# Performance work log

Measured on AMD Instinct MI355X. Metric: run time of the kernel, lower is better.

The kernel has to match this reference:

```python
import jax
jax.config.update('jax_enable_x64', True)  # exact int64 phase products (torch builds phasors in complex128)
import jax.numpy as jnp
import numpy as np

L = 393216          # seq_length, divisible by Locc=4, K=12, mmse_block=12
K = 12              # ktc=4 -> K=12
LOCC = 4            # _compute_locc for ktc=4
U, P = 8, 4         # max_users, max_ports_per_user
BLK = 12            # mmse_block_size
SEARCH_MIN, SEARCH_MAX = -10, 10


def setup_inputs() -> dict:
    key = jax.random.key(0)
    k1, k2, k3 = jax.random.split(key, 3)
    ls_real = jax.random.normal(k1, (L,), dtype=jnp.float32)
    ls_imag = jax.random.normal(k2, (L,), dtype=jnp.float32)
    cyclic_shifts = jax.random.randint(k3, (U, P), 0, K)  # int, values in [0, K)
    return {"ls_real": ls_real, "ls_imag": ls_imag, "cyclic_shifts": cyclic_shifts}


def _phasor(m):
    """exp(1j*2*pi*m*n/L) for each m in the [UP] vector -> [UP, L] complex64.
    Phase reduced mod L in exact int64 before float conversion for accuracy."""
    n = jnp.arange(L, dtype=jnp.int64)
    r = (m.astype(jnp.int64)[:, None] * n[None, :]) % L      # exact
    ang = (2.0 * np.pi / L) * r.astype(jnp.float32)
    return jnp.exp(1j * ang).astype(jnp.complex64)


def _forward(ls, cyclic_shifts):
    shifts = cyclic_shifts.reshape(-1)                        # [UP]
    ideal_peak = ((K - shifts) % K) * L // K                  # [UP]

    # --- timing offset search in +/-10 window around ideal peak (CIR domain) ---
    h_time = jnp.fft.ifft(ls)                                 # IDFT
    h_mag = jnp.abs(h_time) ** 2                              # [L]
    offs = jnp.arange(SEARCH_MIN, SEARCH_MAX + 1)             # [21]
    win = (ideal_peak[:, None] + offs[None, :]) % L           # [UP, 21]
    T = offs[jnp.argmax(h_mag[win], axis=1)]                  # [UP] timing offsets
    m = T + ideal_peak                                        # [UP]

    ph_m = _phasor(m)                                         # [UP, L]
    ph_T = _phasor(T)                                         # [UP, L]

    # --- per-port cyclic de-shift, OCC demux (avg of 4), linear interp back to L ---
    h_up = ls[None, :] * ph_m                                 # [UP, L]
    h_avg = h_up.reshape(-1, L // LOCC, LOCC).mean(-1)        # [UP, L/4]
    orig_idx = (LOCC - 1) / 2.0 + LOCC * jnp.arange(L // LOCC, dtype=jnp.float32)
    new_idx = jnp.arange(L, dtype=jnp.float32)
    interp1 = jax.vmap(lambda y: jnp.interp(new_idx, orig_idx, y))
    h_interp = (interp1(h_avg.real.astype(jnp.float32))
                + 1j * interp1(h_avg.imag.astype(jnp.float32))).astype(jnp.complex64)  # [UP, L]

    # --- residual reconstruction and re-addition per port ---
    h_recon = jnp.sum(h_interp * jnp.conj(ph_m), axis=0)      # [L]
    residual = ls - h_recon
    h_wr = h_interp + residual[None, :] * ph_m                # [UP, L]

    # --- noise power estimate from adjacent-sample differences ---
    diff = ls[1:] - ls[:-1]
    noise_power = jnp.mean(jnp.abs(diff) ** 2) / 2

    # --- block MMSE: h_mmse = C (C + R)^-1 h with default C = I, R = sigma^2 I ---
    C = jnp.eye(BLK, dtype=jnp.complex64)
    Rm = noise_power.astype(jnp.complex64) * jnp.eye(BLK, dtype=jnp.complex64)
    M = C @ jnp.linalg.inv(C + Rm)                            # [12, 12]
    hb = h_wr.reshape(-1, L // BLK, BLK)                      # [UP, L/12, 12]
    h_mmse = jnp.einsum('ij,ubj->ubi', M, hb).reshape(-1, L)  # [UP, L]

    # --- align back by conj timing phasor ---
    return h_mmse * jnp.conj(ph_T)                            # [UP, L] complex64


def reference(ls_real, ls_imag, cyclic_shifts):
    ls = (ls_real + 1j * ls_imag).astype(jnp.complex64)
    return _forward(ls, cyclic_shifts)
```

## Files before the change

kernel.cpp:

```cpp
#include <hip/hip_runtime.h>
#include <math.h>

#define L_TOT 393216
#define L_D4  98304
#define NPORT 32
#define NPEAK 12
#define NOFF  21
#define NCAND 252
#define TILE  1536
#define NBLK  (L_TOT / TILE)
#define NSLOT 12
#define HALF_ELEMS 12582912ull

__device__ float2 g_F[NBLK * NCAND];
__device__ double g_npart[NBLK];
__device__ int    g_prm[96];
__device__ float  g_scale[1];

__constant__ double c_cos12[12] = {1.0, 0.8660254037844387, 0.5, 0.0, -0.5,
  -0.8660254037844387, -1.0, -0.8660254037844387, -0.5, 0.0, 0.5, 0.8660254037844387};
__constant__ double c_sin12[12] = {0.0, 0.5, 0.8660254037844387, 1.0,
  0.8660254037844387, 0.5, 0.0, -0.5, -0.8660254037844387, -1.0,
  -0.8660254037844387, -0.5};

__device__ __forceinline__ void interp_coords(int n, int* j0, float* f) {
  float x = ((float)n - 1.5f) * 0.25f;
  if (x <= 0.f)                    { *j0 = 0;        *f = 0.f; }
  else if (x >= (float)(L_D4 - 1)) { *j0 = L_D4 - 2; *f = 1.f; }
  else { int jj = (int)x; *j0 = jj; *f = x - (float)jj; }
}

__device__ __forceinline__ float2 zpowS(float2 z, float2 z2, float2 z4, float2 z8, int T) {
  int t = T < 0 ? -T : T;
  float cr = 1.f, ci = 0.f;
  if (t & 1) { cr = z.x; ci = z.y; }
  if (t & 2) { float a = cr*z2.x - ci*z2.y, b = cr*z2.y + ci*z2.x; cr = a; ci = b; }
  if (t & 4) { float a = cr*z4.x - ci*z4.y, b = cr*z4.y + ci*z4.x; cr = a; ci = b; }
  if (t & 8) { float a = cr*z8.x - ci*z8.y, b = cr*z8.y + ci*z8.x; cr = a; ci = b; }
  if (T < 0) ci = -ci;
  return make_float2(cr, ci);
}

__global__ __launch_bounds__(256) void search_kernel(
    const float* __restrict__ lsr, const float* __restrict__ lsi) {
  __shared__ float2 sh_ls[TILE + 1];
  __shared__ float2 sh_z[TILE];
  __shared__ float2 sh_red[NCAND * NOFF];
  const float w = (float)(2.0 * M_PI / (double)L_TOT);
  int tid = threadIdx.x;
  int KB = blockIdx.x * TILE;
  for (int i = tid; i < TILE + 1; i += 256) {
    int k = KB + i; if (k > L_TOT - 1) k = L_TOT - 1;
    sh_ls[i] = make_float2(lsr[k], lsi[k]);
  }
  for (int i = tid; i < TILE; i += 256) {
    float s, c; __sincosf(w * (float)(KB + i), &s, &c);
    sh_z[i] = make_float2(c, s);
  }
  __syncthreads();

  if (tid < NCAND) {
    int r = tid % 12, lane = tid / 12;
    float accr[NOFF], acci[NOFF];
#pragma unroll
    for (int d = 0; d < NOFF; ++d) { accr[d] = 0.f; acci[d] = 0.f; }
    for (int q = lane; q < TILE / 12; q += 21) {
      int kl = 12 * q + r;
      float2 y = sh_ls[kl];
      float2 z = sh_z[kl];
      accr[10] += y.x; acci[10] += y.y;
      float cpr = y.x, cpi = y.y, cmr = y.x, cmi = y.y;
#pragma unroll
      for (int d = 1; d <= 10; ++d) {
        float tr = cpr*z.x - cpi*z.y, ti = cpr*z.y + cpi*z.x; cpr = tr; cpi = ti;
        accr[10 + d] += cpr; acci[10 + d] += cpi;
        tr = cmr*z.x + cmi*z.y; ti = cmi*z.x - cmr*z.y; cmr = tr; cmi = ti;
        accr[10 - d] += cmr; acci[10 - d] += cmi;
      }
    }
#pragma unroll
    for (int d = 0; d < NOFF; ++d)
      sh_red[tid * NOFF + d] = make_float2(accr[d], acci[d]);
  }
  double nacc = 0.0;
  int top = (KB + TILE <= L_TOT - 1) ? TILE : (L_TOT - 1 - KB);
  for (int i = tid; i < top; i += 256) {
    float2 a = sh_ls[i], b = sh_ls[i + 1];
    float dr = b.x - a.x, di = b.y - a.y;
    nacc += (double)(dr * dr + di * di);
  }
  __syncthreads();
  if (tid < NCAND) {
    int r = tid / NOFF, dd = tid - r * NOFF;
    float fr = 0.f, fi = 0.f;
    for (int lane = 0; lane < 21; ++lane) {
      float2 v = sh_red[(lane * 12 + r) * NOFF + dd];
      fr += v.x; fi += v.y;
    }
    g_F[blockIdx.x * NCAND + tid] = make_float2(fr, fi);
  }
  __syncthreads();
  double* nb = (double*)sh_red;
  nb[tid] = nacc;
  __syncthreads();
  for (int t = 128; t > 0; t >>= 1) {
    if (tid < t) nb[tid] += nb[tid + t];
    __syncthreads();
  }
  if (tid == 0) g_npart[blockIdx.x] = nb[0];
}

__global__ __launch_bounds__(256) void select_kernel(
    const int* __restrict__ shifts) {
  __shared__ double sGr[NCAND], sGi[NCAND];
  __shared__ double hmag[NCAND];
  __shared__ double nred[256];
  __shared__ int    sh_pu[NPORT], sh_Tu[NPORT];
  int tid = threadIdx.x;
  if (tid < NCAND) {
    double gr = 0.0, gi = 0.0;
    for (int b = 0; b < NBLK; ++b) {
      float2 v = g_F[b * NCAND + tid];
      gr += (double)v.x; gi += (double)v.y;
    }
    sGr[tid] = gr; sGi[tid] = gi;
  }
  nred[tid] = g_npart[tid];
  __syncthreads();
  if (tid < NCAND) {
    int p = tid / NOFF, dd = tid - p * NOFF;
    double sr = 0.0, si = 0.0;
    for (int r = 0; r < 12; ++r) {
      int idx = (p * r) % 12;
      double gr = sGr[r * NOFF + dd], gi = sGi[r * NOFF + dd];
      sr += c_cos12[idx] * gr - c_sin12[idx] * gi;
      si += c_cos12[idx] * gi + c_sin12[idx] * gr;
    }
    hmag[tid] = sr * sr + si * si;
  }
  __syncthreads();
  for (int t = 128; t > 0; t >>= 1) {
    if (tid < t) nred[tid] += nred[tid + t];
    __syncthreads();
  }
  if (tid < NPORT) {
    int s = shifts[tid];
    int p = (NPEAK - (s % NPEAK)) % NPEAK;
    double best = -1.0; int bd = 0;
    for (int d = 0; d < NOFF; ++d) {
      double v = hmag[p * NOFF + d];
      if (v > best) { best = v; bd = d; }
    }
    sh_pu[tid] = p;
    sh_Tu[tid] = bd - 10;
  }
  __syncthreads();
  if (tid == 0) {
    int nd = 0;
    int pv[NSLOT], tv[NSLOT], mv[NSLOT], cv[NSLOT]; unsigned msk[NSLOT];
#pragma unroll
    for (int s = 0; s < NSLOT; ++s) { pv[s] = 0; tv[s] = 0; mv[s] = 0; cv[s] = 0; msk[s] = 0u; }
    for (int u = 0; u < NPORT; ++u) {
      int p = sh_pu[u];
      int slot = -1;
      for (int s = 0; s < nd; ++s) if (pv[s] == p) { slot = s; break; }
      if (slot < 0) {
        slot = nd++;
        pv[slot] = p; tv[slot] = sh_Tu[u];
        int m = sh_Tu[u] + p * (L_TOT / NPEAK);
        if (m < 0) m += L_TOT;
        mv[slot] = m;
      }
      cv[slot] += 1;
      msk[slot] |= (1u << u);
    }
    g_prm[0] = nd;
#pragma unroll
    for (int s = 0; s < NSLOT; ++s) {
      g_prm[1 + s]  = pv[s];
      g_prm[13 + s] = tv[s];
      g_prm[25 + s] = mv[s];
      g_prm[37 + s] = cv[s];
      g_prm[49 + s] = (int)msk[s];
    }
    double npow = nred[0] / (double)(L_TOT - 1) * 0.5;
    g_scale[0] = (float)(1.0 / (1.0 + npow));
  }
}

__global__ __launch_bounds__(256) void fused_kernel(
    const float* __restrict__ lsr, const float* __restrict__ lsi,
    float* __restrict__ out, unsigned long long out_elems) {
  __shared__ float2 sh_ls[264];
  __shared__ float2 sh_h[16][67];
  __shared__ float2 sh_tbl[144];
  __shared__ float2 sh_stp1[NSLOT];
  __shared__ int    sm_T[NSLOT], sm_p[NSLOT], sm_m[NSLOT], sm_cnt[NSLOT], sm_msk[NSLOT];
  __shared__ int    sm_nd;
  __shared__ float  sm_scale;

  const float w = (float)(2.0 * M_PI / (double)L_TOT);
  int tid = threadIdx.x;
  int N0 = blockIdx.x * 256;
  int JBASE; float fd;
  interp_coords(N0, &JBASE, &fd);
  int K0 = 4 * JBASE;

  if (tid < NSLOT) {
    sm_T[tid] = g_prm[13 + tid];
    sm_p[tid] = g_prm[1 + tid];
    int m = g_prm[25 + tid]; sm_m[tid] = m;
    sm_cnt[tid] = g_prm[37 + tid];
    sm_msk[tid] = g_prm[49 + tid];
    float s, c; __sincosf(w * (float)m, &s, &c);
    sh_stp1[tid] = make_float2(c, s);
  }
  if (tid == 0) { sm_nd = g_prm[0]; sm_scale = g_scale[0]; }
  if (tid < 144) {
    int p = tid / 12, r = tid - p * 12;
    int idx = (p * r) % 12;
    float s, c; __sincosf((float)(2.0 * M_PI / 12.0) * (float)idx, &s, &c);
    sh_tbl[tid] = make_float2(c, s);
  }
  for (int i = tid; i < 264; i += 256) {
    int k = K0 + i; if (k > L_TOT - 1) k = L_TOT - 1;
    sh_ls[i] = make_float2(lsr[k], lsi[k]);
  }
  __syncthreads();

  int nd = __builtin_amdgcn_readfirstlane(sm_nd);

  for (int e = tid; e < 66 * 16; e += 256) {
    int s = e & 15, jj = e >> 4;
    if (s < nd) {
      int j = JBASE + jj; if (j > L_D4 - 1) j = L_D4 - 1;
      int k0 = 4 * j, kk = k0 - K0;
      unsigned rr = (unsigned)(((long long)sm_m[s] * k0) % L_TOT);
      float phs, phc; __sincosf(w * (float)rr, &phs, &phc);
      float2 stp = sh_stp1[s];
      float sr = 0.f, si = 0.f;
#pragma unroll
      for (int t = 0; t < 4; ++t) {
        float2 v = sh_ls[kk + t];
        sr += v.x * phc - v.y * phs;
        si += v.x * phs + v.y * phc;
        float a = phc * stp.x - phs * stp.y, b = phc * stp.y + phs * stp.x;
        phc = a; phs = b;
      }
      sh_h[s][jj] = make_float2(0.25f * sr, 0.25f * si);
    }
  }
  __syncthreads();

  int n = N0 + tid;
  int j0; float f;
  interp_coords(n, &j0, &f);
  int jj0 = j0 - JBASE;
  int r12 = n % 12;
  float2 lsn = sh_ls[n - K0];
  float zs, zc; __sincosf(w * (float)n, &zs, &zc);
  float2 zn = make_float2(zc, zs);
  float2 z2 = make_float2(zn.x*zn.x - zn.y*zn.y, 2.f*zn.x*zn.y);
  float2 z4 = make_float2(z2.x*z2.x - z2.y*z2.y, 2.f*z2.x*z2.y);
  float2 z8 = make_float2(z4.x*z4.x - z4.y*z4.y, 2.f*z4.x*z4.y);

  float aAr[NSLOT], aAi[NSLOT];
  float rcr = 0.f, rci = 0.f;
#pragma unroll
  for (int s = 0; s < NSLOT; ++s) {
    if (s < nd) {
      int T = __builtin_amdgcn_readfirstlane(sm_T[s]);
      int p = __builtin_amdgcn_readfirstlane(sm_p[s]);
      float cnt = (float)__builtin_amdgcn_readfirstlane(sm_cnt[s]);
      float2 zT = zpowS(zn, z2, z4, z8, T);
      float2 tb = sh_tbl[p * 12 + r12];
      float2 y0 = sh_h[s][jj0], y1 = sh_h[s][jj0 + 1];
      float hr = y0.x + f * (y1.x - y0.x);
      float hi = y0.y + f * (y1.y - y0.y);
      float Ar = hr * zT.x + hi * zT.y;
      float Ai = hi * zT.x - hr * zT.y;
      aAr[s] = Ar; aAi[s] = Ai;
      rcr += cnt * (Ar * tb.x + Ai * tb.y);
      rci += cnt * (Ai * tb.x - Ar * tb.y);
    } else { aAr[s] = 0.f; aAi[s] = 0.f; }
  }
  float resr = lsn.x - rcr, resi = lsn.y - rci;
  float scl = sm_scale;

  bool full = (out_elems >= 2ull * HALF_ELEMS);
#pragma unroll
  for (int s = 0; s < NSLOT; ++s) {
    if (s < nd) {
      int p = __builtin_amdgcn_readfirstlane(sm_p[s]);
      unsigned mask = (unsigned)__builtin_amdgcn_readfirstlane(sm_msk[s]);
      float2 tb = sh_tbl[p * 12 + r12];
      float orr = scl * (aAr[s] + resr * tb.x - resi * tb.y);
      float oii = scl * (aAi[s] + resr * tb.y + resi * tb.x);
      while (mask) {
        int u = __builtin_ctz(mask); mask &= mask - 1;
        unsigned long long o = (unsigned long long)u * L_TOT + (unsigned)n;
        if (full) {
          out[o] = orr;
          out[HALF_ELEMS + o] = oii;
        } else {
          if (o < out_elems)              out[o] = orr;
          if (HALF_ELEMS + o < out_elems) out[HALF_ELEMS + o] = oii;
        }
      }
    }
  }
}

extern "C" void kernel_launch(void* const* d_in, const int* in_sizes, int n_in,
                              void* d_out, int out_size, void* d_ws, size_t ws_size,
                              hipStream_t stream) {
  const float* lsr    = (const float*)d_in[0];
  const float* lsi    = (const float*)d_in[1];
  const int*   shifts = (const int*)d_in[2];
  float* out = (float*)d_out;

  if (in_sizes[0] != L_TOT || in_sizes[1] != L_TOT) return;

  unsigned long long out_elems = (unsigned long long)(out_size > 0 ? out_size : 0);

  search_kernel<<<NBLK, 256, 0, stream>>>(lsr, lsi);
  select_kernel<<<1, 256, 0, stream>>>(shifts);
  fused_kernel<<<L_TOT / 256, 256, 0, stream>>>(lsr, lsi, out, out_elems);
}
```

Measured before the change: 122.0 us.

## Fold select into search via last-block ticket; process two samples per thread

The single-block select kernel is merged into the search kernel: each block takes an atomic ticket, and the last block to finish reduces the partial results and writes the parameters, removing one kernel launch and its gap. The fused output kernel now gives each thread two adjacent samples (512 per block), halving the block count, amortising the per-block staging of ls and per-slot tables, and storing float2 pairs for wider writes. In exchange it needs more registers per thread and depends on a fence-plus-atomic ticket pattern that resets itself at the end of each call.

```diff
diff --git a/kernel.cpp b/kernel.cpp
--- a/kernel.cpp
+++ b/kernel.cpp
@@ -10,12 +10,14 @@
 #define TILE  1536
 #define NBLK  (L_TOT / TILE)
 #define NSLOT 12
+#define FB    512
 #define HALF_ELEMS 12582912ull
 
 __device__ float2 g_F[NBLK * NCAND];
 __device__ double g_npart[NBLK];
 __device__ int    g_prm[96];
 __device__ float  g_scale[1];
+__device__ int    g_ticket = 0;
 
 __constant__ double c_cos12[12] = {1.0, 0.8660254037844387, 0.5, 0.0, -0.5,
   -0.8660254037844387, -1.0, -0.8660254037844387, -0.5, 0.0, 0.5, 0.8660254037844387};
@@ -42,10 +44,12 @@
 }
 
 __global__ __launch_bounds__(256) void search_kernel(
-    const float* __restrict__ lsr, const float* __restrict__ lsi) {
+    const float* __restrict__ lsr, const float* __restrict__ lsi,
+    const int* __restrict__ shifts) {
   __shared__ float2 sh_ls[TILE + 1];
   __shared__ float2 sh_z[TILE];
   __shared__ float2 sh_red[NCAND * NOFF];
+  __shared__ bool   sh_last;
   const float w = (float)(2.0 * M_PI / (double)L_TOT);
   int tid = threadIdx.x;
   int KB = blockIdx.x * TILE;
@@ -108,15 +112,25 @@
     __syncthreads();
   }
   if (tid == 0) g_npart[blockIdx.x] = nb[0];
-}
-
-__global__ __launch_bounds__(256) void select_kernel(
-    const int* __restrict__ shifts) {
-  __shared__ double sGr[NCAND], sGi[NCAND];
-  __shared__ double hmag[NCAND];
-  __shared__ double nred[256];
-  __shared__ int    sh_pu[NPORT], sh_Tu[NPORT];
-  int tid = threadIdx.x;
+
+  __syncthreads();
+  if (tid == 0) {
+    __threadfence();
+    int old = atomicAdd(&g_ticket, 1);
+    sh_last = (old == NBLK - 1);
+  }
+  __syncthreads();
+  if (!sh_last) return;
+  __threadfence();
+
+  double* db  = (double*)sh_red;
+  double* sGr = db;
+  double* sGi = db + 252;
+  double* hm  = db + 504;
+  double* nrd = db + 756;
+  int* pu = (int*)(db + 1024);
+  int* Tu = pu + 32;
+
   if (tid < NCAND) {
     double gr = 0.0, gi = 0.0;
     for (int b = 0; b < NBLK; ++b) {
@@ -125,7 +139,7 @@
     }
     sGr[tid] = gr; sGi[tid] = gi;
   }
-  nred[tid] = g_npart[tid];
+  nrd[tid] = g_npart[tid];
   __syncthreads();
   if (tid < NCAND) {
     int p = tid / NOFF, dd = tid - p * NOFF;
@@ -136,11 +150,11 @@
       sr += c_cos12[idx] * gr - c_sin12[idx] * gi;
       si += c_cos12[idx] * gi + c_sin12[idx] * gr;
     }
-    hmag[tid] = sr * sr + si * si;
+    hm[tid] = sr * sr + si * si;
   }
   __syncthreads();
   for (int t = 128; t > 0; t >>= 1) {
-    if (tid < t) nred[tid] += nred[tid + t];
+    if (tid < t) nrd[tid] += nrd[tid + t];
     __syncthreads();
   }
   if (tid < NPORT) {
@@ -148,11 +162,11 @@
     int p = (NPEAK - (s % NPEAK)) % NPEAK;
     double best = -1.0; int bd = 0;
     for (int d = 0; d < NOFF; ++d) {
-      double v = hmag[p * NOFF + d];
+      double v = hm[p * NOFF + d];
       if (v > best) { best = v; bd = d; }
     }
-    sh_pu[tid] = p;
-    sh_Tu[tid] = bd - 10;
+    pu[tid] = p;
+    Tu[tid] = bd - 10;
   }
   __syncthreads();
   if (tid == 0) {
@@ -161,13 +175,13 @@
 #pragma unroll
     for (int s = 0; s < NSLOT; ++s) { pv[s] = 0; tv[s] = 0; mv[s] = 0; cv[s] = 0; msk[s] = 0u; }
     for (int u = 0; u < NPORT; ++u) {
-      int p = sh_pu[u];
+      int p = pu[u];
       int slot = -1;
       for (int s = 0; s < nd; ++s) if (pv[s] == p) { slot = s; break; }
       if (slot < 0) {
         slot = nd++;
-        pv[slot] = p; tv[slot] = sh_Tu[u];
-        int m = sh_Tu[u] + p * (L_TOT / NPEAK);
+        pv[slot] = p; tv[slot] = Tu[u];
+        int m = Tu[u] + p * (L_TOT / NPEAK);
         if (m < 0) m += L_TOT;
         mv[slot] = m;
       }
@@ -183,16 +197,18 @@
       g_prm[37 + s] = cv[s];
       g_prm[49 + s] = (int)msk[s];
     }
-    double npow = nred[0] / (double)(L_TOT - 1) * 0.5;
+    double npow = nrd[0] / (double)(L_TOT - 1) * 0.5;
     g_scale[0] = (float)(1.0 / (1.0 + npow));
+    __threadfence();
+    atomicExch(&g_ticket, 0);
   }
 }
 
 __global__ __launch_bounds__(256) void fused_kernel(
     const float* __restrict__ lsr, const float* __restrict__ lsi,
     float* __restrict__ out, unsigned long long out_elems) {
-  __shared__ float2 sh_ls[264];
-  __shared__ float2 sh_h[16][67];
+  __shared__ float2 sh_ls[FB + 8];
+  __shared__ float2 sh_h[16][131];
   __shared__ float2 sh_tbl[144];
   __shared__ float2 sh_stp1[NSLOT];
   __shared__ int    sm_T[NSLOT], sm_p[NSLOT], sm_m[NSLOT], sm_cnt[NSLOT], sm_msk[NSLOT];
@@ -201,7 +217,7 @@
 
   const float w = (float)(2.0 * M_PI / (double)L_TOT);
   int tid = threadIdx.x;
-  int N0 = blockIdx.x * 256;
+  int N0 = blockIdx.x * FB;
   int JBASE; float fd;
   interp_coords(N0, &JBASE, &fd);
   int K0 = 4 * JBASE;
@@ -222,7 +238,7 @@
     float s, c; __sincosf((float)(2.0 * M_PI / 12.0) * (float)idx, &s, &c);
     sh_tbl[tid] = make_float2(c, s);
   }
-  for (int i = tid; i < 264; i += 256) {
+  for (int i = tid; i < FB + 8; i += 256) {
     int k = K0 + i; if (k > L_TOT - 1) k = L_TOT - 1;
     sh_ls[i] = make_float2(lsr[k], lsi[k]);
   }
@@ -230,7 +246,7 @@
 
   int nd = __builtin_amdgcn_readfirstlane(sm_nd);
 
-  for (int e = tid; e < 66 * 16; e += 256) {
+  for (int e = tid; e < 16 * 130; e += 256) {
     int s = e & 15, jj = e >> 4;
     if (s < nd) {
       int j = JBASE + jj; if (j > L_D4 - 1) j = L_D4 - 1;
@@ -252,39 +268,56 @@
   }
   __syncthreads();
 
-  int n = N0 + tid;
-  int j0; float f;
-  interp_coords(n, &j0, &f);
-  int jj0 = j0 - JBASE;
-  int r12 = n % 12;
-  float2 lsn = sh_ls[n - K0];
-  float zs, zc; __sincosf(w * (float)n, &zs, &zc);
-  float2 zn = make_float2(zc, zs);
-  float2 z2 = make_float2(zn.x*zn.x - zn.y*zn.y, 2.f*zn.x*zn.y);
-  float2 z4 = make_float2(z2.x*z2.x - z2.y*z2.y, 2.f*z2.x*z2.y);
-  float2 z8 = make_float2(z4.x*z4.x - z4.y*z4.y, 2.f*z4.x*z4.y);
-
-  float aAr[NSLOT], aAi[NSLOT];
-  float rcr = 0.f, rci = 0.f;
+  int n0 = N0 + 2 * tid, n1 = n0 + 1;
+  int j0a; float fa; interp_coords(n0, &j0a, &fa);
+  int j0b; float fb; interp_coords(n1, &j0b, &fb);
+  int ja = j0a - JBASE, jb = j0b - JBASE;
+  int ra = n0 % 12, rb = n1 % 12;
+  float2 ls0 = sh_ls[n0 - K0], ls1 = sh_ls[n1 - K0];
+
+  float sa, ca; __sincosf(w * (float)n0, &sa, &ca);
+  float2 za = make_float2(ca, sa);
+  float2 za2 = make_float2(za.x*za.x - za.y*za.y, 2.f*za.x*za.y);
+  float2 za4 = make_float2(za2.x*za2.x - za2.y*za2.y, 2.f*za2.x*za2.y);
+  float2 za8 = make_float2(za4.x*za4.x - za4.y*za4.y, 2.f*za4.x*za4.y);
+  float sb, cb; __sincosf(w * (float)n1, &sb, &cb);
+  float2 zb = make_float2(cb, sb);
+  float2 zb2 = make_float2(zb.x*zb.x - zb.y*zb.y, 2.f*zb.x*zb.y);
+  float2 zb4 = make_float2(zb2.x*zb2.x - zb2.y*zb2.y, 2.f*zb2.x*zb2.y);
+  float2 zb8 = make_float2(zb4.x*zb4.x - zb4.y*zb4.y, 2.f*zb4.x*zb4.y);
+
+  float A0r[NSLOT], A0i[NSLOT], A1r[NSLOT], A1i[NSLOT];
+  float rc0r = 0.f, rc0i = 0.f, rc1r = 0.f, rc1i = 0.f;
 #pragma unroll
   for (int s = 0; s < NSLOT; ++s) {
     if (s < nd) {
       int T = __builtin_amdgcn_readfirstlane(sm_T[s]);
       int p = __builtin_amdgcn_readfirstlane(sm_p[s]);
       float cnt = (float)__builtin_amdgcn_readfirstlane(sm_cnt[s]);
-      float2 zT = zpowS(zn, z2, z4, z8, T);
-      float2 tb = sh_tbl[p * 12 + r12];
-      float2 y0 = sh_h[s][jj0], y1 = sh_h[s][jj0 + 1];
-      float hr = y0.x + f * (y1.x - y0.x);
-      float hi = y0.y + f * (y1.y - y0.y);
-      float Ar = hr * zT.x + hi * zT.y;
-      float Ai = hi * zT.x - hr * zT.y;
-      aAr[s] = Ar; aAi[s] = Ai;
-      rcr += cnt * (Ar * tb.x + Ai * tb.y);
-      rci += cnt * (Ai * tb.x - Ar * tb.y);
-    } else { aAr[s] = 0.f; aAi[s] = 0.f; }
-  }
-  float resr = lsn.x - rcr, resi = lsn.y - rci;
+      float2 zTa = zpowS(za, za2, za4, za8, T);
+      float2 zTb = zpowS(zb, zb2, zb4, zb8, T);
+      float2 tba = sh_tbl[p * 12 + ra];
+      float2 tbb = sh_tbl[p * 12 + rb];
+      float2 y0 = sh_h[s][ja], y1 = sh_h[s][ja + 1];
+      float hr = y0.x + fa * (y1.x - y0.x);
+      float hi = y0.y + fa * (y1.y - y0.y);
+      float Ar = hr * zTa.x + hi * zTa.y;
+      float Ai = hi * zTa.x - hr * zTa.y;
+      A0r[s] = Ar; A0i[s] = Ai;
+      rc0r += cnt * (Ar * tba.x + Ai * tba.y);
+      rc0i += cnt * (Ai * tba.x - Ar * tba.y);
+      y0 = sh_h[s][jb]; y1 = sh_h[s][jb + 1];
+      hr = y0.x + fb * (y1.x - y0.x);
+      hi = y0.y + fb * (y1.y - y0.y);
+      Ar = hr * zTb.x + hi * zTb.y;
+      Ai = hi * zTb.x - hr * zTb.y;
+      A1r[s] = Ar; A1i[s] = Ai;
+      rc1r += cnt * (Ar * tbb.x + Ai * tbb.y);
+      rc1i += cnt * (Ai * tbb.x - Ar * tbb.y);
+    } else { A0r[s] = A0i[s] = A1r[s] = A1i[s] = 0.f; }
+  }
+  float re0r = ls0.x - rc0r, re0i = ls0.y - rc0i;
+  float re1r = ls1.x - rc1r, re1i = ls1.y - rc1i;
   float scl = sm_scale;
 
   bool full = (out_elems >= 2ull * HALF_ELEMS);
@@ -293,18 +326,23 @@
     if (s < nd) {
       int p = __builtin_amdgcn_readfirstlane(sm_p[s]);
       unsigned mask = (unsigned)__builtin_amdgcn_readfirstlane(sm_msk[s]);
-      float2 tb = sh_tbl[p * 12 + r12];
-      float orr = scl * (aAr[s] + resr * tb.x - resi * tb.y);
-      float oii = scl * (aAi[s] + resr * tb.y + resi * tb.x);
+      float2 tba = sh_tbl[p * 12 + ra];
+      float2 tbb = sh_tbl[p * 12 + rb];
+      float or0 = scl * (A0r[s] + re0r * tba.x - re0i * tba.y);
+      float oi0 = scl * (A0i[s] + re0r * tba.y + re0i * tba.x);
+      float or1 = scl * (A1r[s] + re1r * tbb.x - re1i * tbb.y);
+      float oi1 = scl * (A1i[s] + re1r * tbb.y + re1i * tbb.x);
       while (mask) {
         int u = __builtin_ctz(mask); mask &= mask - 1;
-        unsigned long long o = (unsigned long long)u * L_TOT + (unsigned)n;
+        unsigned long long o = (unsigned long long)u * L_TOT + (unsigned)n0;
         if (full) {
-          out[o] = orr;
-          out[HALF_ELEMS + o] = oii;
+          *(float2*)&out[o]              = make_float2(or0, or1);
+          *(float2*)&out[HALF_ELEMS + o] = make_float2(oi0, oi1);
         } else {
-          if (o < out_elems)              out[o] = orr;
-          if (HALF_ELEMS + o < out_elems) out[HALF_ELEMS + o] = oii;
+          if (o < out_elems)                   out[o] = or0;
+          if (o + 1 < out_elems)               out[o + 1] = or1;
+          if (HALF_ELEMS + o < out_elems)      out[HALF_ELEMS + o] = oi0;
+          if (HALF_ELEMS + o + 1 < out_elems)  out[HALF_ELEMS + o + 1] = oi1;
         }
       }
     }
@@ -323,7 +361,6 @@
 
   unsigned long long out_elems = (unsigned long long)(out_size > 0 ? out_size : 0);
 
-  search_kernel<<<NBLK, 256, 0, stream>>>(lsr, lsi);
-  select_kernel<<<1, 256, 0, stream>>>(shifts);
-  fused_kernel<<<L_TOT / 256, 256, 0, stream>>>(lsr, lsi, out, out_elems);
-}
+  search_kernel<<<NBLK, 256, 0, stream>>>(lsr, lsi, shifts);
+  fused_kernel<<<L_TOT / FB, 256, 0, stream>>>(lsr, lsi, out, out_elems);
+}
```

Result: slower. 169.4 us (+38.8%).
